# Kernel tuning notes

Measured on AMD Instinct MI355X. Metric: run time of the kernel, lower is better.

The kernel has to match this reference:

```python
import jax, jax.numpy as jnp
import numpy as np

EPS = 1e-6
H = 12  # heads

def layernorm(x, alpha, bias):
    # Faithful to source: unbiased std (ddof=1) and division by (std + eps)
    mean = jnp.mean(x, axis=-1, keepdims=True)
    std = jnp.std(x, axis=-1, ddof=1, keepdims=True)
    return alpha * (x - mean) / (std + EPS) + bias

def setup_inputs() -> dict:
    key = jax.random.key(0)
    ks = jax.random.split(key, 8)
    B, S, D, F = 2, 2048, 768, 3072
    w_scale = 0.02  # keep activations in a sane range
    return {
        "x": jax.random.normal(ks[0], (B, S, D), dtype=jnp.float32),
        "src_mask": jnp.ones((B, 1, 1, S), dtype=jnp.int32),
        "wq": jax.random.normal(ks[1], (D, D), dtype=jnp.float32) * w_scale,
        "wk": jax.random.normal(ks[2], (D, D), dtype=jnp.float32) * w_scale,
        "wv": jax.random.normal(ks[3], (D, D), dtype=jnp.float32) * w_scale,
        "wo": jax.random.normal(ks[4], (D, D), dtype=jnp.float32) * w_scale,
        "w1": jax.random.normal(ks[5], (D, F), dtype=jnp.float32) * w_scale,
        "b1": jnp.zeros((F,), dtype=jnp.float32),
        "w2": jax.random.normal(ks[6], (F, D), dtype=jnp.float32) * w_scale,
        "b2": jnp.zeros((D,), dtype=jnp.float32),
        "ln1_alpha": jnp.ones((1,), dtype=jnp.float32),
        "ln1_bias": jnp.zeros((1,), dtype=jnp.float32),
        "ln2_alpha": jnp.ones((1,), dtype=jnp.float32),
        "ln2_bias": jnp.zeros((1,), dtype=jnp.float32),
    }

def reference(x, src_mask, wq, wk, wv, wo, w1, b1, w2, b2,
              ln1_alpha, ln1_bias, ln2_alpha, ln2_bias):
    B, S, D = x.shape
    dk = D // H
    # ---- residual 1: pre-LN self-attention ----
    t = layernorm(x, ln1_alpha, ln1_bias)
    q = (t @ wq).reshape(B, S, H, dk).transpose(0, 2, 1, 3)  # [B,H,S,dk]
    k = (t @ wk).reshape(B, S, H, dk).transpose(0, 2, 1, 3)
    v = (t @ wv).reshape(B, S, H, dk).transpose(0, 2, 1, 3)
    scores = jnp.einsum('bhqd,bhkd->bhqk', q, k) / jnp.sqrt(jnp.float32(dk))
    # Faithful to source quirk: masked positions are SET to 1e-9 (not -inf)
    scores = jnp.where(src_mask == 0, jnp.float32(1e-9), scores)
    attn = jax.nn.softmax(scores, axis=-1)
    o = jnp.einsum('bhqk,bhkd->bhqd', attn, v)
    o = o.transpose(0, 2, 1, 3).reshape(B, S, D) @ wo
    x = x + o
    # ---- residual 2: pre-LN FFN ----
    t = layernorm(x, ln2_alpha, ln2_bias)
    ffn = jax.nn.relu(t @ w1 + b1) @ w2 + b2
    return x + ffn
```

## Files before the change

### kernel.cpp

```cpp
#include <hip/hip_runtime.h>

typedef float f32x4 __attribute__((ext_vector_type(4)));
typedef __bf16 bf16x8 __attribute__((ext_vector_type(8)));

__device__ __forceinline__ unsigned short f2bf(float f) {
    union { float f; unsigned u; } v; v.f = f;
    unsigned r = v.u + 0x7fffu + ((v.u >> 16) & 1u);
    return (unsigned short)(r >> 16);
}

#define AS1 __attribute__((address_space(1)))
#define AS3 __attribute__((address_space(3)))
__device__ __forceinline__ void async16(const void* g, void* l) {
    __builtin_amdgcn_global_load_lds((AS1 void*)g, (AS3 void*)l, 16, 0, 0);
}

__device__ __forceinline__ void sync_lds() {
    asm volatile("s_waitcnt lgkmcnt(0)\n\ts_barrier" ::: "memory");
}

#define SWZ4(r) ((((r) & 3) ^ (((r) >> 2) & 3)))

__global__ void transpose_cvt(const float* __restrict__ W, unsigned short* __restrict__ Wt,
                              int K, int N) {
    __shared__ float tile[32][33];
    int n0 = blockIdx.x * 32, k0 = blockIdx.y * 32;
    int tx = threadIdx.x, ty = threadIdx.y;
#pragma unroll
    for (int i = 0; i < 32; i += 8)
        tile[ty + i][tx] = W[(size_t)(k0 + ty + i) * N + n0 + tx];
    __syncthreads();
#pragma unroll
    for (int i = 0; i < 32; i += 8)
        Wt[(size_t)(n0 + ty + i) * K + k0 + tx] = f2bf(tile[tx][ty + i]);
}

__global__ __launch_bounds__(256) void ln_kernel(const float* __restrict__ x,
                                                 unsigned short* __restrict__ t,
                                                 const float* __restrict__ alpha,
                                                 const float* __restrict__ bias) {
    const int row = blockIdx.x;
    const float* xr = x + (size_t)row * 768;
    float v[3], sum = 0.f, ss = 0.f;
#pragma unroll
    for (int i = 0; i < 3; i++) {
        v[i] = xr[threadIdx.x + 256 * i];
        sum += v[i]; ss += v[i] * v[i];
    }
#pragma unroll
    for (int off = 32; off; off >>= 1) {
        sum += __shfl_down(sum, off);
        ss  += __shfl_down(ss, off);
    }
    __shared__ float s1[4], s2[4];
    int wid = threadIdx.x >> 6, lane = threadIdx.x & 63;
    if (lane == 0) { s1[wid] = sum; s2[wid] = ss; }
    __syncthreads();
    if (threadIdx.x == 0) {
        float a = 0.f, b = 0.f;
#pragma unroll
        for (int i = 0; i < 4; i++) { a += s1[i]; b += s2[i]; }
        s1[0] = a; s2[0] = b;
    }
    __syncthreads();
    sum = s1[0]; ss = s2[0];
    float mean = sum * (1.f / 768.f);
    float var = (ss - sum * mean) * (1.f / 767.f);
    float sc = alpha[0] / (sqrtf(fmaxf(var, 0.f)) + 1e-6f);
    float bs = bias[0];
#pragma unroll
    for (int i = 0; i < 3; i++)
        t[(size_t)row * 768 + threadIdx.x + 256 * i] = f2bf(sc * (v[i] - mean) + bs);
}

template <int MODE>
__global__ __launch_bounds__(256, 3) void gemm_bt(
    const unsigned short* __restrict__ A, const unsigned short* __restrict__ Bt,
    int M, int N, int K, const float* __restrict__ bias,
    const float* __restrict__ res, void* __restrict__ outp) {
    __shared__ __align__(16) unsigned short As[2][128 * 32];
    __shared__ __align__(16) unsigned short Bs[2][128 * 32];
    const int tid = threadIdx.x;
    const int lane = tid & 63, w = tid >> 6;
    const int wm = w & 1, wn = w >> 1;
    const int m0 = blockIdx.y * 128, n0 = blockIdx.x * 128;
    const int quad = lane >> 4, l16 = lane & 15;

    const int r0 = tid >> 2, g0 = tid & 3;
    const int r1 = r0 + 64, g1 = g0;
    const unsigned short* gA0 = A  + (size_t)(m0 + r0) * K + g0 * 8;
    const unsigned short* gA1 = A  + (size_t)(m0 + r1) * K + g1 * 8;
    const unsigned short* gB0 = Bt + (size_t)(n0 + r0) * K + g0 * 8;
    const unsigned short* gB1 = Bt + (size_t)(n0 + r1) * K + g1 * 8;
    const int wA0 = r0 * 32 + ((g0 ^ SWZ4(r0)) * 8);
    const int wA1 = r1 * 32 + ((g1 ^ SWZ4(r1)) * 8);

    f32x4 acc[4][4];
    const f32x4 z = {0.f, 0.f, 0.f, 0.f};
#pragma unroll
    for (int mt = 0; mt < 4; mt++)
#pragma unroll
        for (int nt = 0; nt < 4; nt++) acc[mt][nt] = z;

    bf16x8 ra0 = *(const bf16x8*)gA0, ra1 = *(const bf16x8*)gA1;
    bf16x8 rb0 = *(const bf16x8*)gB0, rb1 = *(const bf16x8*)gB1;
    gA0 += 32; gA1 += 32; gB0 += 32; gB1 += 32;

    const int nK = K >> 5;
    for (int kt = 0; kt < nK; ++kt) {
        unsigned short* Ac = As[kt & 1];
        unsigned short* Bc = Bs[kt & 1];
        *(bf16x8*)&Ac[wA0] = ra0; *(bf16x8*)&Ac[wA1] = ra1;
        *(bf16x8*)&Bc[wA0] = rb0; *(bf16x8*)&Bc[wA1] = rb1;
        if (kt + 1 < nK) {
            ra0 = *(const bf16x8*)gA0; ra1 = *(const bf16x8*)gA1;
            rb0 = *(const bf16x8*)gB0; rb1 = *(const bf16x8*)gB1;
            gA0 += 32; gA1 += 32; gB0 += 32; gB1 += 32;
        }
        sync_lds();
        bf16x8 af[4], bf[4];
#pragma unroll
        for (int mt = 0; mt < 4; mt++) {
            int r = 64 * wm + 16 * mt + l16;
            af[mt] = *(const bf16x8*)&Ac[r * 32 + ((quad ^ SWZ4(r)) * 8)];
        }
#pragma unroll
        for (int nt = 0; nt < 4; nt++) {
            int r = 64 * wn + 16 * nt + l16;
            bf[nt] = *(const bf16x8*)&Bc[r * 32 + ((quad ^ SWZ4(r)) * 8)];
        }
#pragma unroll
        for (int mt = 0; mt < 4; mt++)
#pragma unroll
            for (int nt = 0; nt < 4; nt++)
                acc[mt][nt] = __builtin_amdgcn_mfma_f32_16x16x32_bf16(af[mt], bf[nt], acc[mt][nt], 0, 0, 0);
    }

#pragma unroll
    for (int mt = 0; mt < 4; mt++) {
#pragma unroll
        for (int nt = 0; nt < 4; nt++) {
            const int col = n0 + 64 * wn + 16 * nt + l16;
            float bv = 0.f;
            if (MODE == 1 || MODE == 3) bv = bias[col];
#pragma unroll
            for (int r = 0; r < 4; r++) {
                const int row = m0 + 64 * wm + 16 * mt + quad * 4 + r;
                const size_t idx = (size_t)row * N + col;
                const float v = acc[mt][nt][r];
                if (MODE == 0) ((unsigned short*)outp)[idx] = f2bf(v);
                else if (MODE == 1) ((unsigned short*)outp)[idx] = f2bf(fmaxf(v + bv, 0.f));
                else if (MODE == 2) ((float*)outp)[idx] = v + res[idx];
                else ((float*)outp)[idx] = v + bv + res[idx];
            }
        }
    }
}

template <int MODE>
__global__ __launch_bounds__(256, 3) void gemm64_bt(
    const unsigned short* __restrict__ A, const unsigned short* __restrict__ Bt,
    int M, int N, int K, const float* __restrict__ bias,
    const float* __restrict__ res, void* __restrict__ outp) {
    __shared__ __align__(16) unsigned short As[2][64 * 64];
    __shared__ __align__(16) unsigned short Bs[2][64 * 64];
    const int tid = threadIdx.x;
    const int lane = tid & 63, w = tid >> 6;
    const int m0 = blockIdx.y * 64, n0 = blockIdx.x * 64;
    const int quad = lane >> 4, l16 = lane & 15;

    const int r0 = tid >> 3, g0 = tid & 7;
    const int r1 = r0 + 32, g1 = g0;
    const unsigned short* gA0 = A  + (size_t)(m0 + r0) * K + g0 * 8;
    const unsigned short* gA1 = A  + (size_t)(m0 + r1) * K + g1 * 8;
    const unsigned short* gB0 = Bt + (size_t)(n0 + r0) * K + g0 * 8;
    const unsigned short* gB1 = Bt + (size_t)(n0 + r1) * K + g1 * 8;
    const int wA0 = r0 * 64 + ((g0 ^ (r0 & 7)) * 8);
    const int wA1 = r1 * 64 + ((g1 ^ (r1 & 7)) * 8);

    f32x4 acc[4];
    const f32x4 z = {0.f, 0.f, 0.f, 0.f};
#pragma unroll
    for (int nt = 0; nt < 4; nt++) acc[nt] = z;

    bf16x8 ra0 = *(const bf16x8*)gA0, ra1 = *(const bf16x8*)gA1;
    bf16x8 rb0 = *(const bf16x8*)gB0, rb1 = *(const bf16x8*)gB1;
    gA0 += 64; gA1 += 64; gB0 += 64; gB1 += 64;

    const int nK = K >> 6;
    for (int kt = 0; kt < nK; ++kt) {
        unsigned short* Ac = As[kt & 1];
        unsigned short* Bc = Bs[kt & 1];
        *(bf16x8*)&Ac[wA0] = ra0; *(bf16x8*)&Ac[wA1] = ra1;
        *(bf16x8*)&Bc[wA0] = rb0; *(bf16x8*)&Bc[wA1] = rb1;
        if (kt + 1 < nK) {
            ra0 = *(const bf16x8*)gA0; ra1 = *(const bf16x8*)gA1;
            rb0 = *(const bf16x8*)gB0; rb1 = *(const bf16x8*)gB1;
            gA0 += 64; gA1 += 64; gB0 += 64; gB1 += 64;
        }
        sync_lds();
        const int ra = 16 * w + l16;
        bf16x8 af0 = *(const bf16x8*)&Ac[ra * 64 + (((0 + quad) ^ (ra & 7)) * 8)];
        bf16x8 af1 = *(const bf16x8*)&Ac[ra * 64 + (((4 + quad) ^ (ra & 7)) * 8)];
#pragma unroll
        for (int nt = 0; nt < 4; nt++) {
            int rb = 16 * nt + l16;
            bf16x8 bf0 = *(const bf16x8*)&Bc[rb * 64 + (((0 + quad) ^ (rb & 7)) * 8)];
            bf16x8 bf1 = *(const bf16x8*)&Bc[rb * 64 + (((4 + quad) ^ (rb & 7)) * 8)];
            acc[nt] = __builtin_amdgcn_mfma_f32_16x16x32_bf16(af0, bf0, acc[nt], 0, 0, 0);
            acc[nt] = __builtin_amdgcn_mfma_f32_16x16x32_bf16(af1, bf1, acc[nt], 0, 0, 0);
        }
    }

#pragma unroll
    for (int nt = 0; nt < 4; nt++) {
        const int col = n0 + 16 * nt + l16;
        float bv = 0.f;
        if (MODE == 1 || MODE == 3) bv = bias[col];
#pragma unroll
        for (int rr = 0; rr < 4; rr++) {
            const int row = m0 + 16 * w + quad * 4 + rr;
            const size_t idx = (size_t)row * N + col;
            const float v = acc[nt][rr];
            if (MODE == 0) ((unsigned short*)outp)[idx] = f2bf(v);
            else if (MODE == 1) ((unsigned short*)outp)[idx] = f2bf(fmaxf(v + bv, 0.f));
            else if (MODE == 2) ((float*)outp)[idx] = v + res[idx];
            else ((float*)outp)[idx] = v + bv + res[idx];
        }
    }
}

__global__ void v_transpose(const unsigned short* __restrict__ qkvc,
                            unsigned short* __restrict__ vt) {
    __shared__ unsigned short t[64][65];
    const int bh = blockIdx.y, b = bh / 12, h = bh % 12;
    const int s0 = blockIdx.x * 64;
    const int tx = threadIdx.x, ty = threadIdx.y;
#pragma unroll
    for (int i = 0; i < 64; i += 4)
        t[ty + i][tx] = qkvc[(size_t)(b * 2048 + s0 + ty + i) * 2304 + 1536 + h * 64 + tx];
    __syncthreads();
#pragma unroll
    for (int i = 0; i < 64; i += 4)
        vt[((size_t)bh * 64 + ty + i) * 2048 + s0 + tx] = t[tx][ty + i];
}

__global__ __launch_bounds__(256, 3) void flash_attn(
    const unsigned short* __restrict__ qkvc,
    const unsigned short* __restrict__ vt,
    const int* __restrict__ mask,
    unsigned short* __restrict__ attno) {
    const int bh = blockIdx.y, b = bh / 12, h = bh % 12;
    const int s0 = blockIdx.x * 64;
    __shared__ __align__(16) unsigned short UQP[4 * 64 * 40];
    __shared__ __align__(16) unsigned short Ks[128 * 64];
    __shared__ __align__(16) unsigned short Vs[64 * 128];
    __shared__ int Ms[128];
    const int tid = threadIdx.x, lane = tid & 63, w = tid >> 6;
    const int quad = lane >> 4, l16 = lane & 15;

    {
        int sl0 = (2 * w) * 64 + lane;
        int r0 = sl0 >> 3, g0 = sl0 & 7;
        int sl1 = sl0 + 64;
        int r1 = sl1 >> 3, g1 = sl1 & 7;
        async16(qkvc + (size_t)(b * 2048 + s0 + r0) * 2304 + h * 64 + ((g0 ^ (r0 & 7)) * 8),
                UQP + (2 * w) * 512);
        async16(qkvc + (size_t)(b * 2048 + s0 + r1) * 2304 + h * 64 + ((g1 ^ (r1 & 7)) * 8),
                UQP + (2 * w + 1) * 512);
    }
    __syncthreads();
    bf16x8 aQ[4][2];
#pragma unroll
    for (int mt = 0; mt < 4; mt++) {
        int r = 16 * mt + l16;
#pragma unroll
        for (int kk = 0; kk < 2; kk++)
            aQ[mt][kk] = *(const bf16x8*)&UQP[r * 64 + (((kk * 4 + quad) ^ (r & 7)) * 8)];
    }
    __bf16* Ps = (__bf16*)UQP + w * (64 * 40);

    f32x4 Oacc[4][4], Lacc[4];
    const f32x4 z = {0.f, 0.f, 0.f, 0.f};
#pragma unroll
    for (int mt = 0; mt < 4; mt++) {
        Lacc[mt] = z;
#pragma unroll
        for (int nt = 0; nt < 4; nt++) Oacc[mt][nt] = z;
    }
    bf16x8 ones;
#pragma unroll
    for (int i = 0; i < 8; i++) ones[i] = (__bf16)1.0f;

    const unsigned short* kbase = qkvc + 768;
    const unsigned short* vbase = vt + (size_t)bh * 64 * 2048;
    const float SCL = 0.125f * 1.44269504088896340736f;
    const float MSK = 1.4426950408889634e-9f;

    for (int j = 0; j < 16; j++) {
        const int k0 = j * 128;
        __syncthreads();
#pragma unroll
        for (int c = 0; c < 4; c++) {
            int sl = (4 * w + c) * 64 + lane;
            int r = sl >> 3, g = sl & 7;
            async16(kbase + (size_t)(b * 2048 + k0 + r) * 2304 + h * 64 + ((g ^ (r & 7)) * 8),
                    Ks + (4 * w + c) * 512);
        }
#pragma unroll
        for (int c = 0; c < 4; c++) {
            int sl = (4 * w + c) * 64 + lane;
            int r = sl >> 4, g = sl & 15;
            async16(vbase + (size_t)r * 2048 + k0 + ((g ^ (r & 15)) * 8),
                    Vs + (4 * w + c) * 512);
        }
        if (tid < 128) Ms[tid] = mask[b * 2048 + k0 + tid];
        __syncthreads();

        f32x4 sc[4][2];
#pragma unroll
        for (int nt = 0; nt < 2; nt++) {
            const int rr = w * 32 + nt * 16 + l16;
            bf16x8 bk0 = *(const bf16x8*)&Ks[rr * 64 + (((0 + quad) ^ (rr & 7)) * 8)];
            bf16x8 bk1 = *(const bf16x8*)&Ks[rr * 64 + (((4 + quad) ^ (rr & 7)) * 8)];
#pragma unroll
            for (int mt = 0; mt < 4; mt++) {
                f32x4 t0 = __builtin_amdgcn_mfma_f32_16x16x32_bf16(aQ[mt][0], bk0, z, 0, 0, 0);
                sc[mt][nt] = __builtin_amdgcn_mfma_f32_16x16x32_bf16(aQ[mt][1], bk1, t0, 0, 0, 0);
            }
        }
#pragma unroll
        for (int nt = 0; nt < 2; nt++) {
            const int msk = Ms[w * 32 + nt * 16 + l16];
            const float fs = msk ? SCL : 0.f;
            const float ad = msk ? 0.f : MSK;
#pragma unroll
            for (int mt = 0; mt < 4; mt++)
#pragma unroll
                for (int r = 0; r < 4; r++)
                    sc[mt][nt][r] = __builtin_amdgcn_exp2f(fmaf(sc[mt][nt][r], fs, ad));
        }
#pragma unroll
        for (int mt = 0; mt < 4; mt++)
#pragma unroll
            for (int nt = 0; nt < 2; nt++)
#pragma unroll
                for (int r = 0; r < 4; r++)
                    Ps[(mt * 16 + quad * 4 + r) * 40 + nt * 16 + l16] = (__bf16)sc[mt][nt][r];

#pragma unroll
        for (int mt = 0; mt < 4; mt++) {
            bf16x8 aP = *(const bf16x8*)&Ps[(mt * 16 + l16) * 40 + quad * 8];
            Lacc[mt] = __builtin_amdgcn_mfma_f32_16x16x32_bf16(aP, ones, Lacc[mt], 0, 0, 0);
#pragma unroll
            for (int nt = 0; nt < 4; nt++) {
                const int rr = nt * 16 + l16;
                bf16x8 bv = *(const bf16x8*)&Vs[rr * 128 + (((w * 4 + quad) ^ (rr & 15)) * 8)];
                Oacc[mt][nt] = __builtin_amdgcn_mfma_f32_16x16x32_bf16(aP, bv, Oacc[mt][nt], 0, 0, 0);
            }
        }
    }

    __syncthreads();
    float* Osc = (float*)Ks;
    float* Lsc = (float*)Vs;
    if (l16 == 0) {
#pragma unroll
        for (int mt = 0; mt < 4; mt++)
#pragma unroll
            for (int r = 0; r < 4; r++)
                Lsc[w * 64 + mt * 16 + quad * 4 + r] = Lacc[mt][r];
    }
#pragma unroll
    for (int mt = 0; mt < 4; mt++) {
#pragma unroll
        for (int nt = 0; nt < 4; nt++)
#pragma unroll
            for (int r = 0; r < 4; r++)
                Osc[(w * 16 + quad * 4 + r) * 64 + nt * 16 + l16] = Oacc[mt][nt][r];
        __syncthreads();
#pragma unroll
        for (int r2 = 0; r2 < 4; r2++) {
            const int lrow = w * 4 + r2;
            float s = Osc[lrow * 64 + lane] + Osc[1024 + lrow * 64 + lane]
                    + Osc[2048 + lrow * 64 + lane] + Osc[3072 + lrow * 64 + lane];
            float L = Lsc[mt * 16 + lrow] + Lsc[64 + mt * 16 + lrow]
                    + Lsc[128 + mt * 16 + lrow] + Lsc[192 + mt * 16 + lrow];
            const int row = s0 + mt * 16 + lrow;
            attno[(size_t)(b * 2048 + row) * 768 + h * 64 + lane] = f2bf(s / L);
        }
        __syncthreads();
    }
}

extern "C" void kernel_launch(void* const* d_in, const int* in_sizes, int n_in,
                              void* d_out, int out_size, void* d_ws, size_t ws_size,
                              hipStream_t stream) {
    const float* x    = (const float*)d_in[0];
    const int*   mask = (const int*)d_in[1];
    const float* wq   = (const float*)d_in[2];
    const float* wk   = (const float*)d_in[3];
    const float* wv   = (const float*)d_in[4];
    const float* wo   = (const float*)d_in[5];
    const float* w1   = (const float*)d_in[6];
    const float* b1   = (const float*)d_in[7];
    const float* w2   = (const float*)d_in[8];
    const float* b2   = (const float*)d_in[9];
    const float* ln1a = (const float*)d_in[10];
    const float* ln1b = (const float*)d_in[11];
    const float* ln2a = (const float*)d_in[12];
    const float* ln2b = (const float*)d_in[13];

    char* p = (char*)d_ws;
    auto carve = [&](size_t bytes) {
        char* q = p;
        p += (bytes + 255) & ~(size_t)255;
        return q;
    };
    unsigned short* wTqkv = (unsigned short*)carve((size_t)2304 * 768 * 2);
    unsigned short* wTo   = (unsigned short*)carve((size_t)768 * 768 * 2);
    unsigned short* wT1   = (unsigned short*)carve((size_t)3072 * 768 * 2);
    unsigned short* wT2   = (unsigned short*)carve((size_t)768 * 3072 * 2);
    unsigned short* vtb   = (unsigned short*)carve((size_t)24 * 64 * 2048 * 2);
    float*          x1    = (float*)carve((size_t)4096 * 768 * 4);
    char* unionA = carve((size_t)4096 * 768 * 2 + (size_t)4096 * 2304 * 2);
    unsigned short* t1   = (unsigned short*)unionA;
    unsigned short* qkvc = (unsigned short*)(unionA + (size_t)4096 * 768 * 2);
    unsigned short* ffnh = (unsigned short*)unionA;
    unsigned short* attno = (unsigned short*)carve((size_t)4096 * 768 * 2);
    unsigned short* t2 = attno;

    dim3 tb(32, 8);
    transpose_cvt<<<dim3(24, 24), tb, 0, stream>>>(wq, wTqkv, 768, 768);
    transpose_cvt<<<dim3(24, 24), tb, 0, stream>>>(wk, wTqkv + (size_t)768 * 768, 768, 768);
    transpose_cvt<<<dim3(24, 24), tb, 0, stream>>>(wv, wTqkv + (size_t)1536 * 768, 768, 768);
    transpose_cvt<<<dim3(24, 24), tb, 0, stream>>>(wo, wTo, 768, 768);
    transpose_cvt<<<dim3(96, 24), tb, 0, stream>>>(w1, wT1, 768, 3072);
    transpose_cvt<<<dim3(24, 96), tb, 0, stream>>>(w2, wT2, 3072, 768);

    ln_kernel<<<4096, 256, 0, stream>>>(x, t1, ln1a, ln1b);
    gemm_bt<0><<<dim3(18, 32), 256, 0, stream>>>(t1, wTqkv, 4096, 2304, 768,
                                                 nullptr, nullptr, qkvc);
    v_transpose<<<dim3(32, 24), dim3(64, 4), 0, stream>>>(qkvc, vtb);
    flash_attn<<<dim3(32, 24), 256, 0, stream>>>(qkvc, vtb, mask, attno);
    gemm64_bt<2><<<dim3(12, 64), 256, 0, stream>>>(attno, wTo, 4096, 768, 768,
                                                   nullptr, x, x1);
    ln_kernel<<<4096, 256, 0, stream>>>(x1, t2, ln2a, ln2b);
    gemm_bt<1><<<dim3(24, 32), 256, 0, stream>>>(t2, wT1, 4096, 3072, 768,
                                                 b1, nullptr, ffnh);
    gemm64_bt<3><<<dim3(12, 64), 256, 0, stream>>>(ffnh, wT2, 4096, 768, 3072,
                                                   b2, x1, (float*)d_out);
}
```

Before: 301.9 us.

## Split flash attention waves 2x2 over queries and keys to shrink accumulators

The four waves in the attention kernel are re-partitioned from a 4-way split over the key block into a 2x2 grid: two query halves times two key halves. Each wave now holds half as many Q fragments and O accumulators, which lowers register pressure, and it fuses the score MFMA, exp2 and P store into one loop. The final reduction now only merges two partial results instead of four, and it writes output straight from registers, removing most of the epilogue barriers and LDS traffic. The cost is an extra barrier after the Q load, because P now aliases Q's LDS, and each wave performs more V fragment reads per key block.

```diff
diff --git a/kernel.cpp b/kernel.cpp
--- a/kernel.cpp
+++ b/kernel.cpp
@@ -252,12 +252,13 @@
     unsigned short* __restrict__ attno) {
     const int bh = blockIdx.y, b = bh / 12, h = bh % 12;
     const int s0 = blockIdx.x * 64;
-    __shared__ __align__(16) unsigned short UQP[4 * 64 * 40];
+    __shared__ __align__(16) unsigned short UQP[4 * 32 * 72];
     __shared__ __align__(16) unsigned short Ks[128 * 64];
     __shared__ __align__(16) unsigned short Vs[64 * 128];
     __shared__ int Ms[128];
     const int tid = threadIdx.x, lane = tid & 63, w = tid >> 6;
     const int quad = lane >> 4, l16 = lane & 15;
+    const int wq = w & 1, wk = w >> 1;
 
     {
         int sl0 = (2 * w) * 64 + lane;
@@ -270,20 +271,21 @@
                 UQP + (2 * w + 1) * 512);
     }
     __syncthreads();
-    bf16x8 aQ[4][2];
-#pragma unroll
-    for (int mt = 0; mt < 4; mt++) {
-        int r = 16 * mt + l16;
+    bf16x8 aQ[2][2];
+#pragma unroll
+    for (int mt = 0; mt < 2; mt++) {
+        int r = wq * 32 + mt * 16 + l16;
 #pragma unroll
         for (int kk = 0; kk < 2; kk++)
             aQ[mt][kk] = *(const bf16x8*)&UQP[r * 64 + (((kk * 4 + quad) ^ (r & 7)) * 8)];
     }
-    __bf16* Ps = (__bf16*)UQP + w * (64 * 40);
-
-    f32x4 Oacc[4][4], Lacc[4];
+    __syncthreads();
+    __bf16* Ps = (__bf16*)UQP + w * (32 * 72);
+
+    f32x4 Oacc[2][4], Lacc[2];
     const f32x4 z = {0.f, 0.f, 0.f, 0.f};
 #pragma unroll
-    for (int mt = 0; mt < 4; mt++) {
+    for (int mt = 0; mt < 2; mt++) {
         Lacc[mt] = z;
 #pragma unroll
         for (int nt = 0; nt < 4; nt++) Oacc[mt][nt] = z;
@@ -317,46 +319,38 @@
         if (tid < 128) Ms[tid] = mask[b * 2048 + k0 + tid];
         __syncthreads();
 
-        f32x4 sc[4][2];
-#pragma unroll
-        for (int nt = 0; nt < 2; nt++) {
-            const int rr = w * 32 + nt * 16 + l16;
+#pragma unroll
+        for (int nt = 0; nt < 4; nt++) {
+            const int rr = wk * 64 + nt * 16 + l16;
             bf16x8 bk0 = *(const bf16x8*)&Ks[rr * 64 + (((0 + quad) ^ (rr & 7)) * 8)];
             bf16x8 bk1 = *(const bf16x8*)&Ks[rr * 64 + (((4 + quad) ^ (rr & 7)) * 8)];
-#pragma unroll
-            for (int mt = 0; mt < 4; mt++) {
-                f32x4 t0 = __builtin_amdgcn_mfma_f32_16x16x32_bf16(aQ[mt][0], bk0, z, 0, 0, 0);
-                sc[mt][nt] = __builtin_amdgcn_mfma_f32_16x16x32_bf16(aQ[mt][1], bk1, t0, 0, 0, 0);
-            }
-        }
-#pragma unroll
-        for (int nt = 0; nt < 2; nt++) {
-            const int msk = Ms[w * 32 + nt * 16 + l16];
+            const int msk = Ms[wk * 64 + nt * 16 + l16];
             const float fs = msk ? SCL : 0.f;
             const float ad = msk ? 0.f : MSK;
 #pragma unroll
-            for (int mt = 0; mt < 4; mt++)
+            for (int mt = 0; mt < 2; mt++) {
+                f32x4 t0 = __builtin_amdgcn_mfma_f32_16x16x32_bf16(aQ[mt][0], bk0, z, 0, 0, 0);
+                f32x4 sc = __builtin_amdgcn_mfma_f32_16x16x32_bf16(aQ[mt][1], bk1, t0, 0, 0, 0);
 #pragma unroll
                 for (int r = 0; r < 4; r++)
-                    sc[mt][nt][r] = __builtin_amdgcn_exp2f(fmaf(sc[mt][nt][r], fs, ad));
-        }
-#pragma unroll
-        for (int mt = 0; mt < 4; mt++)
-#pragma unroll
-            for (int nt = 0; nt < 2; nt++)
-#pragma unroll
-                for (int r = 0; r < 4; r++)
-                    Ps[(mt * 16 + quad * 4 + r) * 40 + nt * 16 + l16] = (__bf16)sc[mt][nt][r];
-
-#pragma unroll
-        for (int mt = 0; mt < 4; mt++) {
-            bf16x8 aP = *(const bf16x8*)&Ps[(mt * 16 + l16) * 40 + quad * 8];
-            Lacc[mt] = __builtin_amdgcn_mfma_f32_16x16x32_bf16(aP, ones, Lacc[mt], 0, 0, 0);
-#pragma unroll
-            for (int nt = 0; nt < 4; nt++) {
-                const int rr = nt * 16 + l16;
-                bf16x8 bv = *(const bf16x8*)&Vs[rr * 128 + (((w * 4 + quad) ^ (rr & 15)) * 8)];
-                Oacc[mt][nt] = __builtin_amdgcn_mfma_f32_16x16x32_bf16(aP, bv, Oacc[mt][nt], 0, 0, 0);
+                    Ps[(mt * 16 + quad * 4 + r) * 72 + nt * 16 + l16] =
+                        (__bf16)__builtin_amdgcn_exp2f(fmaf(sc[r], fs, ad));
+            }
+        }
+
+#pragma unroll
+        for (int kt2 = 0; kt2 < 2; kt2++) {
+#pragma unroll
+            for (int mt = 0; mt < 2; mt++) {
+                bf16x8 aP = *(const bf16x8*)&Ps[(mt * 16 + l16) * 72 + kt2 * 32 + quad * 8];
+                Lacc[mt] = __builtin_amdgcn_mfma_f32_16x16x32_bf16(aP, ones, Lacc[mt], 0, 0, 0);
+#pragma unroll
+                for (int nt = 0; nt < 4; nt++) {
+                    const int rr = nt * 16 + l16;
+                    bf16x8 bv = *(const bf16x8*)&Vs[rr * 128 +
+                                (((wk * 8 + kt2 * 4 + quad) ^ (rr & 15)) * 8)];
+                    Oacc[mt][nt] = __builtin_amdgcn_mfma_f32_16x16x32_bf16(aP, bv, Oacc[mt][nt], 0, 0, 0);
+                }
             }
         }
     }
@@ -364,32 +358,39 @@
     __syncthreads();
     float* Osc = (float*)Ks;
     float* Lsc = (float*)Vs;
-    if (l16 == 0) {
-#pragma unroll
-        for (int mt = 0; mt < 4; mt++)
-#pragma unroll
-            for (int r = 0; r < 4; r++)
-                Lsc[w * 64 + mt * 16 + quad * 4 + r] = Lacc[mt][r];
-    }
-#pragma unroll
-    for (int mt = 0; mt < 4; mt++) {
-#pragma unroll
-        for (int nt = 0; nt < 4; nt++)
-#pragma unroll
-            for (int r = 0; r < 4; r++)
-                Osc[(w * 16 + quad * 4 + r) * 64 + nt * 16 + l16] = Oacc[mt][nt][r];
-        __syncthreads();
-#pragma unroll
-        for (int r2 = 0; r2 < 4; r2++) {
-            const int lrow = w * 4 + r2;
-            float s = Osc[lrow * 64 + lane] + Osc[1024 + lrow * 64 + lane]
-                    + Osc[2048 + lrow * 64 + lane] + Osc[3072 + lrow * 64 + lane];
-            float L = Lsc[mt * 16 + lrow] + Lsc[64 + mt * 16 + lrow]
-                    + Lsc[128 + mt * 16 + lrow] + Lsc[192 + mt * 16 + lrow];
-            const int row = s0 + mt * 16 + lrow;
-            attno[(size_t)(b * 2048 + row) * 768 + h * 64 + lane] = f2bf(s / L);
-        }
-        __syncthreads();
+    if (wk == 1) {
+#pragma unroll
+        for (int mt = 0; mt < 2; mt++) {
+            if (l16 == 0)
+#pragma unroll
+                for (int r = 0; r < 4; r++)
+                    Lsc[wq * 32 + mt * 16 + quad * 4 + r] = Lacc[mt][r];
+#pragma unroll
+            for (int nt = 0; nt < 4; nt++)
+#pragma unroll
+                for (int r = 0; r < 4; r++)
+                    Osc[(size_t)(wq * 32 + mt * 16 + quad * 4 + r) * 64 + nt * 16 + l16] =
+                        Oacc[mt][nt][r];
+        }
+    }
+    __syncthreads();
+    if (wk == 0) {
+#pragma unroll
+        for (int mt = 0; mt < 2; mt++) {
+#pragma unroll
+            for (int r = 0; r < 4; r++) {
+                const int ql = wq * 32 + mt * 16 + quad * 4 + r;
+                const float L = Lacc[mt][r] + Lsc[ql];
+                const float inv = 1.0f / L;
+                const int row = s0 + ql;
+#pragma unroll
+                for (int nt = 0; nt < 4; nt++) {
+                    const float s = Oacc[mt][nt][r] + Osc[(size_t)ql * 64 + nt * 16 + l16];
+                    attno[(size_t)(b * 2048 + row) * 768 + h * 64 + nt * 16 + l16] =
+                        f2bf(s * inv);
+                }
+            }
+        }
     }
 }
 
```

Result: faster. 276.3 us (-8.5%).
